# Kernel optimization log

Hardware: AMD Instinct MI355X
Metric: run time of the kernel (lower is better)

Reference implementation:

```python
import jax, jax.numpy as jnp
import numpy as np

D = 1024
H = 16
DEPTH = D // H


def setup_inputs() -> dict:
    key = jax.random.key(0)
    ks = jax.random.split(key, 9)
    s = 1.0 / np.sqrt(D)
    return {
        "x": jax.random.normal(ks[0], (2, 2048, D), dtype=jnp.float32),
        "Wq": jax.random.uniform(ks[1], (D, D), jnp.float32, -s, s),
        "bq": jax.random.uniform(ks[2], (D,), jnp.float32, -s, s),
        "Wk": jax.random.uniform(ks[3], (D, D), jnp.float32, -s, s),
        "bk": jax.random.uniform(ks[4], (D,), jnp.float32, -s, s),
        "Wv": jax.random.uniform(ks[5], (D, D), jnp.float32, -s, s),
        "bv": jax.random.uniform(ks[6], (D,), jnp.float32, -s, s),
        "Wo": jax.random.uniform(ks[7], (D, D), jnp.float32, -s, s),
        "bo": jax.random.uniform(ks[8], (D,), jnp.float32, -s, s),
    }


def _split_heads(t):
    b, s, _ = t.shape
    return t.reshape(b, s, H, DEPTH).transpose(0, 2, 1, 3)  # [B,H,S,depth]


def reference(x, Wq, bq, Wk, bk, Wv, bv, Wo, bo):
    q = _split_heads(x @ Wq.T + bq)
    k = _split_heads(x @ Wk.T + bk)
    v = _split_heads(x @ Wv.T + bv)
    scores = jnp.einsum("bhqd,bhkd->bhqk", q, k) / jnp.sqrt(jnp.float32(DEPTH))
    weights = jax.nn.softmax(scores, axis=-1)
    attn = jnp.einsum("bhqk,bhkd->bhqd", weights, v)
    b, _, s, _ = attn.shape
    attn = attn.transpose(0, 2, 1, 3).reshape(b, s, D)
    return attn @ Wo.T + bo
```

## Files before the change

kernel.cpp:

```cpp
#include <hip/hip_runtime.h>
#include <hip/hip_bf16.h>


typedef __bf16 bf16x8 __attribute__((ext_vector_type(8)));
typedef float f32x4 __attribute__((ext_vector_type(4)));
typedef unsigned short u16;
typedef unsigned short u16x4 __attribute__((ext_vector_type(4)));
typedef unsigned short u16x8 __attribute__((ext_vector_type(8)));
typedef unsigned int u32x2 __attribute__((ext_vector_type(2)));

__device__ __forceinline__ u16 f2bf(float f) {
  union { float f; unsigned u; } x; x.f = f;
  return (u16)((x.u + 0x7fffu + ((x.u >> 16) & 1u)) >> 16);
}

__device__ __forceinline__ void load_lds16(const void* g, void* l) {
  __builtin_amdgcn_global_load_lds((const __attribute__((address_space(1))) void*)g,
                                   (__attribute__((address_space(3))) void*)l,
                                   16, 0, 0);
}

__device__ __forceinline__ bf16x8 frag128(const u16* base, int row, int ch) {
  return *(const bf16x8*)((const char*)base + row * 128 + (((ch) ^ (row & 7)) << 4));
}
__device__ __forceinline__ bf16x8 frag256(const u16* base, int row, int ch) {
  return *(const bf16x8*)((const char*)base + row * 256 + (((ch) ^ (row & 7)) << 4));
}

__device__ __forceinline__ float exp2_hw(float x) {
  float r;
  asm("v_exp_f32 %0, %1" : "=v"(r) : "v"(x));
  return r;
}

__device__ __forceinline__ unsigned cvt_pk_bf16(float lo, float hi) {
  unsigned r;
  asm("v_cvt_pk_bf16_f32 %0, %1, %2" : "=v"(r) : "v"(lo), "v"(hi));
  return r;
}

__global__ __launch_bounds__(256) void cvt_all(
    const float* __restrict__ x, const float* __restrict__ wq,
    const float* __restrict__ wk, const float* __restrict__ wv,
    const float* __restrict__ wo, u16* __restrict__ dst) {
  int i = blockIdx.x * 256 + threadIdx.x;
  const float* src;
  int loc;
  if (i < 1048576) {
    src = x; loc = i;
  } else {
    int j = i - 1048576;
    int seg = j >> 18;
    loc = j & 262143;
    src = (seg == 0) ? wq : (seg == 1) ? wk : (seg == 2) ? wv : wo;
  }
  f32x4 v = ((const f32x4*)src)[loc];
  u16x4 o;
#pragma unroll
  for (int j = 0; j < 4; ++j) o[j] = f2bf(v[j]);
  ((u16x4*)dst)[i] = o;
}

template <int BM, int MODE>
__global__ __launch_bounds__(256) void gemm_bf16(
    const u16* __restrict__ A, const u16* __restrict__ Bw,
    const float* __restrict__ bias0, const float* __restrict__ bias1,
    const float* __restrict__ bias2,
    u16* __restrict__ o_q, u16* __restrict__ o_k, u16* __restrict__ o_vt,
    float* __restrict__ o_f, int K) {
  constexpr int MBF = BM / 32;
  __shared__ u16 sA[BM * 64];
  __shared__ u16 sB[128 * 64];
  const int tid = threadIdx.x, l = tid & 63, w = tid >> 6;
  const int wr = w >> 1, wc = w & 1;
  const int lr = l & 15, lq = l >> 4;
  const int m0 = blockIdx.y * BM, n0 = blockIdx.x * 128;

  f32x4 acc[MBF][4];
#pragma unroll
  for (int mb = 0; mb < MBF; ++mb)
#pragma unroll
    for (int nb = 0; nb < 4; ++nb) acc[mb][nb] = f32x4{0.f, 0.f, 0.f, 0.f};

  const int nkt = K / 64;
  for (int kt = 0; kt < nkt; ++kt) {
#pragma unroll
    for (int i = 0; i < BM / 32; ++i) {
      int p = (i * 4 + w) * 1024 + l * 16;
      int row = p >> 7, ch = ((p >> 4) & 7) ^ (row & 7);
      load_lds16(A + (size_t)(m0 + row) * K + kt * 64 + ch * 8,
                 (char*)sA + (i * 4 + w) * 1024);
    }
#pragma unroll
    for (int i = 0; i < 4; ++i) {
      int p = (i * 4 + w) * 1024 + l * 16;
      int row = p >> 7, ch = ((p >> 4) & 7) ^ (row & 7);
      load_lds16(Bw + (size_t)(n0 + row) * K + kt * 64 + ch * 8,
                 (char*)sB + (i * 4 + w) * 1024);
    }
    __syncthreads();
#pragma unroll
    for (int ks = 0; ks < 2; ++ks) {
      bf16x8 af[MBF], bfr[4];
#pragma unroll
      for (int mb = 0; mb < MBF; ++mb)
        af[mb] = frag128(sA, wr * (BM / 2) + mb * 16 + lr, lq + 4 * ks);
#pragma unroll
      for (int nb = 0; nb < 4; ++nb)
        bfr[nb] = frag128(sB, wc * 64 + nb * 16 + lr, lq + 4 * ks);
#pragma unroll
      for (int mb = 0; mb < MBF; ++mb)
#pragma unroll
        for (int nb = 0; nb < 4; ++nb)
          acc[mb][nb] = __builtin_amdgcn_mfma_f32_16x16x32_bf16(
              af[mb], bfr[nb], acc[mb][nb], 0, 0, 0);
    }
    __syncthreads();
  }

#pragma unroll
  for (int nb = 0; nb < 4; ++nb) {
    const int n = n0 + wc * 64 + nb * 16 + lr;
    if constexpr (MODE == 0) {
      const int qkv = n >> 10, c = n & 1023;
      const float* bp = (qkv == 0) ? bias0 : ((qkv == 1) ? bias1 : bias2);
      const float bv = bp[c];
      const int h = c >> 6, d = c & 63;
      if (qkv == 2) {
#pragma unroll
        for (int mb = 0; mb < MBF; ++mb) {
          int mbase = m0 + wr * (BM / 2) + mb * 16 + lq * 4;
          int b = mbase >> 11, s0 = mbase & 2047;
          u16x4 pk;
#pragma unroll
          for (int r = 0; r < 4; ++r) pk[r] = f2bf(acc[mb][nb][r] + bv);
          *(u16x4*)(o_vt + ((size_t)((b * 16 + h) * 64 + d)) * 2048 + s0) = pk;
        }
      } else {
        u16* dp = (qkv == 0) ? o_q : o_k;
#pragma unroll
        for (int mb = 0; mb < MBF; ++mb)
#pragma unroll
          for (int r = 0; r < 4; ++r) {
            int m = m0 + wr * (BM / 2) + mb * 16 + lq * 4 + r;
            int b = m >> 11, s = m & 2047;
            float v = acc[mb][nb][r] + bv;
            if (qkv == 0) v *= 0.18033688011f;
            dp[((size_t)(b * 16 + h) * 2048 + s) * 64 + d] = f2bf(v);
          }
      }
    } else {
      const float bv = bias0[n];
#pragma unroll
      for (int mb = 0; mb < MBF; ++mb)
#pragma unroll
        for (int r = 0; r < 4; ++r) {
          int m = m0 + wr * (BM / 2) + mb * 16 + lq * 4 + r;
          o_f[(size_t)m * 1024 + n] = acc[mb][nb][r] + bv;
        }
    }
  }
}

__global__ __launch_bounds__(256, 2) void attn_fwd(
    const u16* __restrict__ q16, const u16* __restrict__ k16,
    const u16* __restrict__ vt16, u16* __restrict__ att16) {
  __shared__ u16 sK[128 * 64];
  __shared__ u16 sV[64 * 128];
  __shared__ u16 sP[4][32 * 64];
  const int tid = threadIdx.x, l = tid & 63, w = tid >> 6;
  const int lr = l & 15, lq = l >> 4;
  const int qt = blockIdx.x, bh = blockIdx.y;
  const int b = bh >> 4, h = bh & 15;
  const char* kg = (const char*)(k16 + (size_t)bh * 2048 * 64);
  const char* vg = (const char*)(vt16 + (size_t)bh * 64 * 2048);
  char* sPw = (char*)&sP[w][0];
  const int swzP = (lr & 7) << 4;

  bf16x8 aq[2][2];
#pragma unroll
  for (int mb = 0; mb < 2; ++mb)
#pragma unroll
    for (int ks = 0; ks < 2; ++ks) {
      int qrow = qt * 128 + w * 32 + mb * 16 + lr;
      aq[mb][ks] = *(const bf16x8*)(q16 + ((size_t)bh * 2048 + qrow) * 64 +
                                    ks * 32 + lq * 8);
    }

  const int krow0 = tid >> 3, kch = tid & 7;
  const int vrow0 = tid >> 4, vch = tid & 15;

  f32x4 kbuf[4], vbuf[4];
#pragma unroll
  for (int j = 0; j < 4; ++j)
    kbuf[j] = *(const f32x4*)(kg + j * 4096 + tid * 16);
#pragma unroll
  for (int j = 0; j < 4; ++j)
    vbuf[j] = *(const f32x4*)(vg + (size_t)(j * 16 + vrow0) * 4096 + vch * 16);

  f32x4 o[2][4];
#pragma unroll
  for (int mb = 0; mb < 2; ++mb)
#pragma unroll
    for (int db = 0; db < 4; ++db) o[mb][db] = f32x4{0.f, 0.f, 0.f, 0.f};
  float l_run[2] = {0.f, 0.f};

  for (int kt = 0; kt < 16; ++kt) {
#pragma unroll
    for (int j = 0; j < 4; ++j) {
      int row = j * 32 + krow0;
      *(f32x4*)((char*)sK + row * 128 + ((kch ^ (row & 7)) << 4)) = kbuf[j];
    }
#pragma unroll
    for (int j = 0; j < 4; ++j) {
      int row = j * 16 + vrow0;
      *(f32x4*)((char*)sV + row * 256 + ((vch ^ (row & 7)) << 4)) = vbuf[j];
    }
    if (kt < 15) {
#pragma unroll
      for (int j = 0; j < 4; ++j)
        kbuf[j] = *(const f32x4*)(kg + (kt + 1) * 16384 + j * 4096 + tid * 16);
#pragma unroll
      for (int j = 0; j < 4; ++j)
        vbuf[j] = *(const f32x4*)(vg + (size_t)(j * 16 + vrow0) * 4096 +
                                  (kt + 1) * 256 + vch * 16);
    }
    __syncthreads();

    f32x4 s[2][8];
#pragma unroll
    for (int mb = 0; mb < 2; ++mb)
#pragma unroll
      for (int nb = 0; nb < 8; ++nb) s[mb][nb] = f32x4{0.f, 0.f, 0.f, 0.f};
    __builtin_amdgcn_s_setprio(1);
#pragma unroll
    for (int ks = 0; ks < 2; ++ks) {
#pragma unroll
      for (int g = 0; g < 2; ++g) {
        bf16x8 bk[4];
#pragma unroll
        for (int j = 0; j < 4; ++j)
          bk[j] = frag128(sK, (g * 4 + j) * 16 + lr, lq + 4 * ks);
#pragma unroll
        for (int j = 0; j < 4; ++j)
#pragma unroll
          for (int mb = 0; mb < 2; ++mb)
            s[mb][g * 4 + j] = __builtin_amdgcn_mfma_f32_16x16x32_bf16(
                bk[j], aq[mb][ks], s[mb][g * 4 + j], 0, 0, 0);
      }
    }
    __builtin_amdgcn_s_setprio(0);

#pragma unroll
    for (int mb = 0; mb < 2; ++mb) {
      float rs = 0.f;
#pragma unroll
      for (int nb = 0; nb < 8; ++nb)
#pragma unroll
        for (int r = 0; r < 4; ++r) {
          float p_ = exp2_hw(s[mb][nb][r]);
          s[mb][nb][r] = p_;
          rs += p_;
        }
      l_run[mb] += rs;
    }

#pragma unroll
    for (int hf = 0; hf < 2; ++hf) {
#pragma unroll
      for (int mb = 0; mb < 2; ++mb) {
        int qrow = mb * 16 + lr;
#pragma unroll
        for (int nb2 = 0; nb2 < 4; ++nb2) {
          u32x2 pk;
          pk[0] = cvt_pk_bf16(s[mb][hf * 4 + nb2][0], s[mb][hf * 4 + nb2][1]);
          pk[1] = cvt_pk_bf16(s[mb][hf * 4 + nb2][2], s[mb][hf * 4 + nb2][3]);
          *(u32x2*)(sPw + qrow * 128 + ((nb2 * 32 + lq * 8) ^ swzP)) = pk;
        }
      }
      __builtin_amdgcn_s_setprio(1);
#pragma unroll
      for (int c2 = 0; c2 < 2; ++c2) {
        bf16x8 ap[2], bv[4];
#pragma unroll
        for (int mb = 0; mb < 2; ++mb)
          ap[mb] = *(const bf16x8*)(sPw + (mb * 16 + lr) * 128 +
                                    ((c2 * 64 + lq * 16) ^ swzP));
#pragma unroll
        for (int db = 0; db < 4; ++db)
          bv[db] = frag256(sV, db * 16 + lr, (hf * 2 + c2) * 4 + lq);
#pragma unroll
        for (int db = 0; db < 4; ++db)
#pragma unroll
          for (int mb = 0; mb < 2; ++mb)
            o[mb][db] = __builtin_amdgcn_mfma_f32_16x16x32_bf16(
                ap[mb], bv[db], o[mb][db], 0, 0, 0);
      }
      __builtin_amdgcn_s_setprio(0);
    }
    __syncthreads();
  }

#pragma unroll
  for (int mb = 0; mb < 2; ++mb) {
    float lv = l_run[mb];
    lv += __shfl_xor(lv, 16, 64);
    lv += __shfl_xor(lv, 32, 64);
    float inv[4];
#pragma unroll
    for (int r = 0; r < 4; ++r) inv[r] = 1.f / __shfl(lv, lq * 4 + r, 64);
#pragma unroll
    for (int db = 0; db < 4; ++db)
#pragma unroll
      for (int r = 0; r < 4; ++r) {
        float v = o[mb][db][r] * inv[r];
        int qg_ = qt * 128 + w * 32 + mb * 16 + lq * 4 + r;
        int col = h * 64 + db * 16 + lr;
        att16[((size_t)(b * 2048 + qg_)) * 1024 + col] = f2bf(v);
      }
  }
}

extern "C" void kernel_launch(void* const* d_in, const int* in_sizes, int n_in,
                              void* d_out, int out_size, void* d_ws, size_t ws_size,
                              hipStream_t stream) {
  const float* x  = (const float*)d_in[0];
  const float* Wq = (const float*)d_in[1];
  const float* bq = (const float*)d_in[2];
  const float* Wk = (const float*)d_in[3];
  const float* bk = (const float*)d_in[4];
  const float* Wv = (const float*)d_in[5];
  const float* bv = (const float*)d_in[6];
  const float* Wo = (const float*)d_in[7];
  const float* bo = (const float*)d_in[8];
  float* out = (float*)d_out;

  char* ws = (char*)d_ws;
  const size_t MB = 1024 * 1024;
  if (ws_size < 40 * MB) return;
  u16* x16  = (u16*)(ws);
  u16* w16  = (u16*)(ws + 8 * MB);
  u16* q16  = (u16*)(ws + 16 * MB);
  u16* k16  = (u16*)(ws + 24 * MB);
  u16* vt16 = (u16*)(ws + 32 * MB);
  u16* att16 = x16;

  cvt_all<<<8192, 256, 0, stream>>>(x, Wq, Wk, Wv, Wo, x16);

  gemm_bf16<128, 0><<<dim3(24, 32), 256, 0, stream>>>(
      x16, w16, bq, bk, bv, q16, k16, vt16, nullptr, 1024);

  attn_fwd<<<dim3(16, 32), 256, 0, stream>>>(q16, k16, vt16, att16);

  gemm_bf16<64, 1><<<dim3(8, 64), 256, 0, stream>>>(
      att16, w16 + 3145728, bo, nullptr, nullptr, nullptr, nullptr, nullptr,
      out, 1024);
}
```

Baseline: 115.6 us.

## Load K and V fragments directly from global memory, drop shared staging

The attention kernel no longer stages K and V tiles through shared memory with register prefetch and block barriers. Each wave now loads its MFMA B-operand fragments straight from global memory (L2/L1), which removes LDS traffic and both __syncthreads per tile. The cost is that all four waves redundantly fetch the same K/V data and there is no explicit prefetch, so latency is exposed unless occupancy hides it. Register pressure also rises because a full tile of fragments is held in registers.

```diff
diff --git a/kernel.cpp b/kernel.cpp
--- a/kernel.cpp
+++ b/kernel.cpp
@@ -22,9 +22,6 @@
 
 __device__ __forceinline__ bf16x8 frag128(const u16* base, int row, int ch) {
   return *(const bf16x8*)((const char*)base + row * 128 + (((ch) ^ (row & 7)) << 4));
-}
-__device__ __forceinline__ bf16x8 frag256(const u16* base, int row, int ch) {
-  return *(const bf16x8*)((const char*)base + row * 256 + (((ch) ^ (row & 7)) << 4));
 }
 
 __device__ __forceinline__ float exp2_hw(float x) {
@@ -165,8 +162,6 @@
 __global__ __launch_bounds__(256, 2) void attn_fwd(
     const u16* __restrict__ q16, const u16* __restrict__ k16,
     const u16* __restrict__ vt16, u16* __restrict__ att16) {
-  __shared__ u16 sK[128 * 64];
-  __shared__ u16 sV[64 * 128];
   __shared__ u16 sP[4][32 * 64];
   const int tid = threadIdx.x, l = tid & 63, w = tid >> 6;
   const int lr = l & 15, lq = l >> 4;
@@ -187,16 +182,8 @@
                                     ks * 32 + lq * 8);
     }
 
-  const int krow0 = tid >> 3, kch = tid & 7;
-  const int vrow0 = tid >> 4, vch = tid & 15;
-
-  f32x4 kbuf[4], vbuf[4];
-#pragma unroll
-  for (int j = 0; j < 4; ++j)
-    kbuf[j] = *(const f32x4*)(kg + j * 4096 + tid * 16);
-#pragma unroll
-  for (int j = 0; j < 4; ++j)
-    vbuf[j] = *(const f32x4*)(vg + (size_t)(j * 16 + vrow0) * 4096 + vch * 16);
+  const char* kfrag = kg + (size_t)lr * 128;
+  const char* vfrag = vg + (size_t)lr * 4096;
 
   f32x4 o[2][4];
 #pragma unroll
@@ -206,26 +193,21 @@
   float l_run[2] = {0.f, 0.f};
 
   for (int kt = 0; kt < 16; ++kt) {
-#pragma unroll
-    for (int j = 0; j < 4; ++j) {
-      int row = j * 32 + krow0;
-      *(f32x4*)((char*)sK + row * 128 + ((kch ^ (row & 7)) << 4)) = kbuf[j];
-    }
-#pragma unroll
-    for (int j = 0; j < 4; ++j) {
-      int row = j * 16 + vrow0;
-      *(f32x4*)((char*)sV + row * 256 + ((vch ^ (row & 7)) << 4)) = vbuf[j];
-    }
-    if (kt < 15) {
-#pragma unroll
-      for (int j = 0; j < 4; ++j)
-        kbuf[j] = *(const f32x4*)(kg + (kt + 1) * 16384 + j * 4096 + tid * 16);
-#pragma unroll
-      for (int j = 0; j < 4; ++j)
-        vbuf[j] = *(const f32x4*)(vg + (size_t)(j * 16 + vrow0) * 4096 +
-                                  (kt + 1) * 256 + vch * 16);
-    }
-    __syncthreads();
+    bf16x8 bk[2][8];
+#pragma unroll
+    for (int ks = 0; ks < 2; ++ks)
+#pragma unroll
+      for (int j8 = 0; j8 < 8; ++j8)
+        bk[ks][j8] = *(const bf16x8*)(kfrag + (size_t)kt * 16384 +
+                                      (size_t)j8 * 2048 +
+                                      (lq + 4 * ks) * 16);
+    bf16x8 bv0[2][4];
+#pragma unroll
+    for (int c2 = 0; c2 < 2; ++c2)
+#pragma unroll
+      for (int db = 0; db < 4; ++db)
+        bv0[c2][db] = *(const bf16x8*)(vfrag + (size_t)db * 65536 +
+                                       kt * 256 + (c2 * 4 + lq) * 16);
 
     f32x4 s[2][8];
 #pragma unroll
@@ -234,21 +216,13 @@
       for (int nb = 0; nb < 8; ++nb) s[mb][nb] = f32x4{0.f, 0.f, 0.f, 0.f};
     __builtin_amdgcn_s_setprio(1);
 #pragma unroll
-    for (int ks = 0; ks < 2; ++ks) {
-#pragma unroll
-      for (int g = 0; g < 2; ++g) {
-        bf16x8 bk[4];
-#pragma unroll
-        for (int j = 0; j < 4; ++j)
-          bk[j] = frag128(sK, (g * 4 + j) * 16 + lr, lq + 4 * ks);
-#pragma unroll
-        for (int j = 0; j < 4; ++j)
-#pragma unroll
-          for (int mb = 0; mb < 2; ++mb)
-            s[mb][g * 4 + j] = __builtin_amdgcn_mfma_f32_16x16x32_bf16(
-                bk[j], aq[mb][ks], s[mb][g * 4 + j], 0, 0, 0);
-      }
-    }
+    for (int ks = 0; ks < 2; ++ks)
+#pragma unroll
+      for (int j8 = 0; j8 < 8; ++j8)
+#pragma unroll
+        for (int mb = 0; mb < 2; ++mb)
+          s[mb][j8] = __builtin_amdgcn_mfma_f32_16x16x32_bf16(
+              bk[ks][j8], aq[mb][ks], s[mb][j8], 0, 0, 0);
     __builtin_amdgcn_s_setprio(0);
 
 #pragma unroll
@@ -266,39 +240,67 @@
     }
 
 #pragma unroll
-    for (int hf = 0; hf < 2; ++hf) {
-#pragma unroll
-      for (int mb = 0; mb < 2; ++mb) {
-        int qrow = mb * 16 + lr;
-#pragma unroll
-        for (int nb2 = 0; nb2 < 4; ++nb2) {
-          u32x2 pk;
-          pk[0] = cvt_pk_bf16(s[mb][hf * 4 + nb2][0], s[mb][hf * 4 + nb2][1]);
-          pk[1] = cvt_pk_bf16(s[mb][hf * 4 + nb2][2], s[mb][hf * 4 + nb2][3]);
-          *(u32x2*)(sPw + qrow * 128 + ((nb2 * 32 + lq * 8) ^ swzP)) = pk;
-        }
+    for (int mb = 0; mb < 2; ++mb) {
+      int qrow = mb * 16 + lr;
+#pragma unroll
+      for (int nb2 = 0; nb2 < 4; ++nb2) {
+        u32x2 pk;
+        pk[0] = cvt_pk_bf16(s[mb][nb2][0], s[mb][nb2][1]);
+        pk[1] = cvt_pk_bf16(s[mb][nb2][2], s[mb][nb2][3]);
+        *(u32x2*)(sPw + qrow * 128 + ((nb2 * 32 + lq * 8) ^ swzP)) = pk;
       }
-      __builtin_amdgcn_s_setprio(1);
-#pragma unroll
-      for (int c2 = 0; c2 < 2; ++c2) {
-        bf16x8 ap[2], bv[4];
+    }
+    bf16x8 bv1[2][4];
+#pragma unroll
+    for (int c2 = 0; c2 < 2; ++c2)
+#pragma unroll
+      for (int db = 0; db < 4; ++db)
+        bv1[c2][db] = *(const bf16x8*)(vfrag + (size_t)db * 65536 +
+                                       kt * 256 + ((2 + c2) * 4 + lq) * 16);
+    __builtin_amdgcn_s_setprio(1);
+#pragma unroll
+    for (int c2 = 0; c2 < 2; ++c2) {
+      bf16x8 ap[2];
+#pragma unroll
+      for (int mb = 0; mb < 2; ++mb)
+        ap[mb] = *(const bf16x8*)(sPw + (mb * 16 + lr) * 128 +
+                                  ((c2 * 64 + lq * 16) ^ swzP));
+#pragma unroll
+      for (int db = 0; db < 4; ++db)
 #pragma unroll
         for (int mb = 0; mb < 2; ++mb)
-          ap[mb] = *(const bf16x8*)(sPw + (mb * 16 + lr) * 128 +
-                                    ((c2 * 64 + lq * 16) ^ swzP));
-#pragma unroll
-        for (int db = 0; db < 4; ++db)
-          bv[db] = frag256(sV, db * 16 + lr, (hf * 2 + c2) * 4 + lq);
-#pragma unroll
-        for (int db = 0; db < 4; ++db)
-#pragma unroll
-          for (int mb = 0; mb < 2; ++mb)
-            o[mb][db] = __builtin_amdgcn_mfma_f32_16x16x32_bf16(
-                ap[mb], bv[db], o[mb][db], 0, 0, 0);
+          o[mb][db] = __builtin_amdgcn_mfma_f32_16x16x32_bf16(
+              ap[mb], bv0[c2][db], o[mb][db], 0, 0, 0);
+    }
+    __builtin_amdgcn_s_setprio(0);
+
+#pragma unroll
+    for (int mb = 0; mb < 2; ++mb) {
+      int qrow = mb * 16 + lr;
+#pragma unroll
+      for (int nb2 = 0; nb2 < 4; ++nb2) {
+        u32x2 pk;
+        pk[0] = cvt_pk_bf16(s[mb][4 + nb2][0], s[mb][4 + nb2][1]);
+        pk[1] = cvt_pk_bf16(s[mb][4 + nb2][2], s[mb][4 + nb2][3]);
+        *(u32x2*)(sPw + qrow * 128 + ((nb2 * 32 + lq * 8) ^ swzP)) = pk;
       }
-      __builtin_amdgcn_s_setprio(0);
-    }
-    __syncthreads();
+    }
+    __builtin_amdgcn_s_setprio(1);
+#pragma unroll
+    for (int c2 = 0; c2 < 2; ++c2) {
+      bf16x8 ap[2];
+#pragma unroll
+      for (int mb = 0; mb < 2; ++mb)
+        ap[mb] = *(const bf16x8*)(sPw + (mb * 16 + lr) * 128 +
+                                  ((c2 * 64 + lq * 16) ^ swzP));
+#pragma unroll
+      for (int db = 0; db < 4; ++db)
+#pragma unroll
+        for (int mb = 0; mb < 2; ++mb)
+          o[mb][db] = __builtin_amdgcn_mfma_f32_16x16x32_bf16(
+              ap[mb], bv1[c2][db], o[mb][db], 0, 0, 0);
+    }
+    __builtin_amdgcn_s_setprio(0);
   }
 
 #pragma unroll
```

Measured after the change: 183.6 us. 1.59x slower.

## Double-buffer K/V tiles in LDS and remap attention block order for locality

Applied to the files above, without the earlier changes.

Attention K and V tiles are now double-buffered in shared memory. The next tile is written to the alternate buffer after compute, and the global prefetch runs two tiles ahead, so each iteration needs one barrier instead of two phases. The block index is also remapped so consecutive workgroups are spread across heads, likely to balance XCD/L2 placement. LDS use per block doubles for K/V (64KB total with sP), which may reduce occupancy below the two blocks per CU the launch bounds request.

```diff
diff --git a/kernel.cpp b/kernel.cpp
--- a/kernel.cpp
+++ b/kernel.cpp
@@ -165,12 +165,14 @@
 __global__ __launch_bounds__(256, 2) void attn_fwd(
     const u16* __restrict__ q16, const u16* __restrict__ k16,
     const u16* __restrict__ vt16, u16* __restrict__ att16) {
-  __shared__ u16 sK[128 * 64];
-  __shared__ u16 sV[64 * 128];
+  __shared__ u16 sK[2][128 * 64];
+  __shared__ u16 sV[2][64 * 128];
   __shared__ u16 sP[4][32 * 64];
   const int tid = threadIdx.x, l = tid & 63, w = tid >> 6;
   const int lr = l & 15, lq = l >> 4;
-  const int qt = blockIdx.x, bh = blockIdx.y;
+  const int lin = (blockIdx.y << 4) | blockIdx.x;
+  const int wg = (lin & 7) * 64 + (lin >> 3);
+  const int qt = wg & 15, bh = wg >> 4;
   const int b = bh >> 4, h = bh & 15;
   const char* kg = (const char*)(k16 + (size_t)bh * 2048 * 64);
   const char* vg = (const char*)(vt16 + (size_t)bh * 64 * 2048);
@@ -197,6 +199,24 @@
 #pragma unroll
   for (int j = 0; j < 4; ++j)
     vbuf[j] = *(const f32x4*)(vg + (size_t)(j * 16 + vrow0) * 4096 + vch * 16);
+#pragma unroll
+  for (int j = 0; j < 4; ++j) {
+    int row = j * 32 + krow0;
+    *(f32x4*)((char*)sK[0] + row * 128 + ((kch ^ (row & 7)) << 4)) = kbuf[j];
+  }
+#pragma unroll
+  for (int j = 0; j < 4; ++j) {
+    int row = j * 16 + vrow0;
+    *(f32x4*)((char*)sV[0] + row * 256 + ((vch ^ (row & 7)) << 4)) = vbuf[j];
+  }
+#pragma unroll
+  for (int j = 0; j < 4; ++j)
+    kbuf[j] = *(const f32x4*)(kg + 16384 + j * 4096 + tid * 16);
+#pragma unroll
+  for (int j = 0; j < 4; ++j)
+    vbuf[j] = *(const f32x4*)(vg + (size_t)(j * 16 + vrow0) * 4096 +
+                              256 + vch * 16);
+  __syncthreads();
 
   f32x4 o[2][4];
 #pragma unroll
@@ -206,26 +226,9 @@
   float l_run[2] = {0.f, 0.f};
 
   for (int kt = 0; kt < 16; ++kt) {
-#pragma unroll
-    for (int j = 0; j < 4; ++j) {
-      int row = j * 32 + krow0;
-      *(f32x4*)((char*)sK + row * 128 + ((kch ^ (row & 7)) << 4)) = kbuf[j];
-    }
-#pragma unroll
-    for (int j = 0; j < 4; ++j) {
-      int row = j * 16 + vrow0;
-      *(f32x4*)((char*)sV + row * 256 + ((vch ^ (row & 7)) << 4)) = vbuf[j];
-    }
-    if (kt < 15) {
-#pragma unroll
-      for (int j = 0; j < 4; ++j)
-        kbuf[j] = *(const f32x4*)(kg + (kt + 1) * 16384 + j * 4096 + tid * 16);
-#pragma unroll
-      for (int j = 0; j < 4; ++j)
-        vbuf[j] = *(const f32x4*)(vg + (size_t)(j * 16 + vrow0) * 4096 +
-                                  (kt + 1) * 256 + vch * 16);
-    }
-    __syncthreads();
+    const int cur = kt & 1;
+    const u16* sKc = sK[cur];
+    const u16* sVc = sV[cur];
 
     f32x4 s[2][8];
 #pragma unroll
@@ -240,7 +243,7 @@
         bf16x8 bk[4];
 #pragma unroll
         for (int j = 0; j < 4; ++j)
-          bk[j] = frag128(sK, (g * 4 + j) * 16 + lr, lq + 4 * ks);
+          bk[j] = frag128(sKc, (g * 4 + j) * 16 + lr, lq + 4 * ks);
 #pragma unroll
         for (int j = 0; j < 4; ++j)
 #pragma unroll
@@ -288,7 +291,7 @@
                                     ((c2 * 64 + lq * 16) ^ swzP));
 #pragma unroll
         for (int db = 0; db < 4; ++db)
-          bv[db] = frag256(sV, db * 16 + lr, (hf * 2 + c2) * 4 + lq);
+          bv[db] = frag256(sVc, db * 16 + lr, (hf * 2 + c2) * 4 + lq);
 #pragma unroll
         for (int db = 0; db < 4; ++db)
 #pragma unroll
@@ -297,6 +300,31 @@
                 ap[mb], bv[db], o[mb][db], 0, 0, 0);
       }
       __builtin_amdgcn_s_setprio(0);
+    }
+
+    if (kt < 15) {
+      u16* sKn = sK[cur ^ 1];
+      u16* sVn = sV[cur ^ 1];
+#pragma unroll
+      for (int j = 0; j < 4; ++j) {
+        int row = j * 32 + krow0;
+        *(f32x4*)((char*)sKn + row * 128 + ((kch ^ (row & 7)) << 4)) = kbuf[j];
+      }
+#pragma unroll
+      for (int j = 0; j < 4; ++j) {
+        int row = j * 16 + vrow0;
+        *(f32x4*)((char*)sVn + row * 256 + ((vch ^ (row & 7)) << 4)) = vbuf[j];
+      }
+      if (kt < 14) {
+#pragma unroll
+        for (int j = 0; j < 4; ++j)
+          kbuf[j] = *(const f32x4*)(kg + (size_t)(kt + 2) * 16384 +
+                                    j * 4096 + tid * 16);
+#pragma unroll
+        for (int j = 0; j < 4; ++j)
+          vbuf[j] = *(const f32x4*)(vg + (size_t)(j * 16 + vrow0) * 4096 +
+                                    (kt + 2) * 256 + vch * 16);
+      }
     }
     __syncthreads();
   }
```

New measurement: 114.9 us. Within noise of the previous version (-0.6%).
